# Kernel tuning notes

Hardware: AMD Instinct MI355X
Metric: run time of the kernel (lower is better)

Reference implementation:

```python
import jax, jax.numpy as jnp
import numpy as np

# FP4 (e2m1) value table: sign bit in code>>3, magnitude in code&7
FP4 = jnp.array([0.0, 0.5, 1.0, 1.5, 2.0, 3.0, 4.0, 6.0,
                 -0.0, -0.5, -1.0, -1.5, -2.0, -3.0, -4.0, -6.0], dtype=jnp.float32)
BLOCK = 32  # MX block size: one shared E8M0 scale per 32 elements


def _unpack(packed):
    # packed: int32 holding byte values 0..255; low nibble first
    lo = packed & 0xF
    hi = (packed >> 4) & 0xF
    return jnp.stack([lo, hi], axis=-1).reshape(*packed.shape[:-1], packed.shape[-1] * 2)


def _dequant(packed, sf):
    # packed: [..., N//2] packed FP4 codes; sf: [..., N//32] E8M0 exponents
    vals = FP4[_unpack(packed)]                       # [..., N]
    n = vals.shape[-1]
    scale = jnp.exp2(sf.astype(jnp.float32) - 127.0)  # [..., N//32]
    vals = vals.reshape(*vals.shape[:-1], n // BLOCK, BLOCK) * scale[..., None]
    return vals.reshape(*scale.shape[:-1], n)


def setup_inputs() -> dict:
    key = jax.random.key(0)
    ks = jax.random.split(key, 6)
    M, IN, OUT, R = 8192, 4096, 4096, 128
    return {
        "x_q": jax.random.randint(ks[0], (M, IN // 2), 0, 256, dtype=jnp.int32),
        "scales_x": jax.random.randint(ks[1], (M, IN // BLOCK), 120, 134, dtype=jnp.int32),
        "weight": jax.random.randint(ks[2], (OUT, IN // 2), 0, 256, dtype=jnp.int32),
        "SF_w": jax.random.randint(ks[3], (OUT * IN // BLOCK,), 120, 134, dtype=jnp.int32),
        "low_rank_weight": jax.random.randint(ks[4], (OUT, R // 2), 0, 256, dtype=jnp.int32),
        "SF_low_rank_weight": jax.random.randint(ks[5], (OUT * R // BLOCK,), 120, 134, dtype=jnp.int32),
    }


def reference(x_q, scales_x, weight, SF_w, low_rank_weight, SF_low_rank_weight):
    OUT = weight.shape[0]
    IN = weight.shape[1] * 2
    R = low_rank_weight.shape[1] * 2  # 128
    # Low-rank path: first R unpacked features of x (R//2 packed bytes, R//32 scale blocks)
    x_lr = _dequant(x_q[:, :R // 2], scales_x[:, :R // BLOCK])                    # [M, R]
    W_lr = _dequant(low_rank_weight, SF_low_rank_weight.reshape(OUT, R // BLOCK))  # [OUT, R]
    out = jnp.einsum('mr,or->mo', x_lr, W_lr, preferred_element_type=jnp.float32)
    # Main 4-bit matmul fused with the low-rank correction
    x = _dequant(x_q, scales_x)                               # [M, IN]
    W = _dequant(weight, SF_w.reshape(OUT, IN // BLOCK))      # [OUT, IN]
    out = out + jnp.einsum('mi,oi->mo', x, W, preferred_element_type=jnp.float32)
    return out
```

## Files before the change

kernel.cpp:

```cpp
#include <hip/hip_runtime.h>
#include <hip/hip_bf16.h>
#include <stdint.h>


#define M_DIM 8192
#define N_DIM 4096
#define K_MAIN 4096
#define K_TOT 4224
#define NCHUNK 132
#define NT 33

#define XP_OFF   ((size_t)0)
#define WP_OFF   (XP_OFF + (size_t)NCHUNK * M_DIM * 16)
#define SXH_OFF  (WP_OFF + (size_t)NCHUNK * N_DIM * 16)
#define SWH_OFF  (SXH_OFF + (size_t)NT * 2 * M_DIM * 2)
#define WS_NEED  (SWH_OFF + (size_t)NT * 2 * N_DIM * 2)

typedef __attribute__((ext_vector_type(4))) float f32x4;
typedef __attribute__((ext_vector_type(16))) float f32x16;
typedef __attribute__((ext_vector_type(8))) short short8;
typedef __attribute__((ext_vector_type(8))) _Float16 half8;
typedef __attribute__((ext_vector_type(4))) int i32x4;
typedef __attribute__((ext_vector_type(8))) int i32x8;

#define SBAR() asm volatile("s_barrier" ::: "memory")

#define PXP_N (NCHUNK * M_DIM)
#define PWP_N (NCHUNK * N_DIM)
#define TSX_N (NT * 2 * M_DIM / 2)
#define TSW_N (NT * 2 * N_DIM / 2)
#define PACK_TOTAL (PXP_N + PWP_N + TSX_N + TSW_N)

__device__ inline unsigned pack4(i32x4 q) {
    return (q.x & 255) | ((q.y & 255) << 8) | ((q.z & 255) << 16) |
           ((unsigned)(q.w & 255) << 24);
}

__global__ __launch_bounds__(256)
void pack_kernel(const int* __restrict__ xq, const int* __restrict__ sx,
                 const int* __restrict__ w, const int* __restrict__ sfw,
                 const int* __restrict__ lrw, const int* __restrict__ sflr,
                 uint8_t* __restrict__ ws) {
    int t = blockIdx.x * 256 + threadIdx.x;
    if (t < PXP_N) {
        const int g = t >> 13;
        const int m = t & 8191;
        const int gs = (g < 128) ? g : (g - 128);
        const int* src = xq + (size_t)m * 2048 + gs * 16;
        i32x4 o;
        o.x = (int)pack4(*(const i32x4*)(src + 0));
        o.y = (int)pack4(*(const i32x4*)(src + 4));
        o.z = (int)pack4(*(const i32x4*)(src + 8));
        o.w = (int)pack4(*(const i32x4*)(src + 12));
        *(i32x4*)(ws + XP_OFF + ((size_t)g * M_DIM + m) * 16) = o;
    } else if (t < PXP_N + PWP_N) {
        const int i = t - PXP_N;
        const int g = i >> 12;
        const int n = i & 4095;
        const int* src = (g < 128) ? (w + (size_t)n * 2048 + g * 16)
                                   : (lrw + (size_t)n * 64 + (g - 128) * 16);
        i32x4 o;
        o.x = (int)pack4(*(const i32x4*)(src + 0));
        o.y = (int)pack4(*(const i32x4*)(src + 4));
        o.z = (int)pack4(*(const i32x4*)(src + 8));
        o.w = (int)pack4(*(const i32x4*)(src + 12));
        *(i32x4*)(ws + WP_OFF + ((size_t)g * N_DIM + n) * 16) = o;
    } else if (t < PXP_N + PWP_N + TSX_N) {
        int i = t - PXP_N - PWP_N;
        int plane = i >> 12;
        int kt = plane >> 1, h = plane & 1;
        int r2 = (i & 4095) << 1;
        int g0 = kt * 4 + h, g2 = g0 + 2;
        int s0 = (g0 < 128) ? g0 : g0 - 128;
        int s2 = (g2 < 128) ? g2 : g2 - 128;
        unsigned b0 = sx[(size_t)r2 * 128 + s0] & 255;
        unsigned b1 = sx[(size_t)r2 * 128 + s2] & 255;
        unsigned b2 = sx[(size_t)(r2 + 1) * 128 + s0] & 255;
        unsigned b3 = sx[(size_t)(r2 + 1) * 128 + s2] & 255;
        *(unsigned*)(ws + SXH_OFF + (size_t)i * 4) = b0 | (b1 << 8) | (b2 << 16) | (b3 << 24);
    } else if (t < PACK_TOTAL) {
        int i = t - PXP_N - PWP_N - TSX_N;
        int plane = i >> 11;
        int kt = plane >> 1, h = plane & 1;
        int r2 = (i & 2047) << 1;
        int g0 = kt * 4 + h, g2 = g0 + 2;
        unsigned b0, b1, b2, b3;
        if (g0 < 128) { b0 = sfw[(size_t)r2 * 128 + g0] & 255; b2 = sfw[(size_t)(r2 + 1) * 128 + g0] & 255; }
        else          { b0 = sflr[(size_t)r2 * 4 + (g0 - 128)] & 255; b2 = sflr[(size_t)(r2 + 1) * 4 + (g0 - 128)] & 255; }
        if (g2 < 128) { b1 = sfw[(size_t)r2 * 128 + g2] & 255; b3 = sfw[(size_t)(r2 + 1) * 128 + g2] & 255; }
        else          { b1 = sflr[(size_t)r2 * 4 + (g2 - 128)] & 255; b3 = sflr[(size_t)(r2 + 1) * 4 + (g2 - 128)] & 255; }
        *(unsigned*)(ws + SWH_OFF + (size_t)i * 4) = b0 | (b1 << 8) | (b2 << 16) | (b3 << 24);
    }
}

__device__ inline void gload_lds16(const void* g, void* l) {
    __builtin_amdgcn_global_load_lds(
        (const __attribute__((address_space(1))) unsigned int*)g,
        (__attribute__((address_space(3))) unsigned int*)l, 16, 0, 0);
}

__device__ inline i32x8 ext8(i32x4 v) {
    return __builtin_shufflevector(v, v, 0, 1, 2, 3, -1, -1, -1, -1);
}

__global__ __launch_bounds__(512, 2)
void l4b_mx8(const uint8_t* __restrict__ xp, const uint8_t* __restrict__ wp,
             const uint8_t* __restrict__ sxH, const uint8_t* __restrict__ swH,
             float* __restrict__ out) {
    __shared__ __align__(16) uint8_t As[3][4][256][16];
    __shared__ __align__(16) uint8_t Bs[3][4][256][16];

    const int tid = threadIdx.x;
    const int lane = tid & 63;
    const int wid = tid >> 6;
    const int wr = wid >> 2;
    const int wc = wid & 3;

    const int bid = blockIdx.x;
    const int wgid = (bid & 7) * 64 + (bid >> 3);
    const int bn = (wgid & 15) * 256;
    const int bm = (wgid >> 4) * 256;

    const int h = lane >> 5, r = lane & 31;

    const int cst = wid & 3;
    const uint8_t* ga = (wid < 4)
        ? xp + ((size_t)cst * M_DIM + bm + lane) * 16
        : wp + ((size_t)cst * N_DIM + bn + lane) * 16;
    const size_t gstride = (wid < 4) ? (size_t)4 * M_DIM * 16 : (size_t)4 * N_DIM * 16;
    const uint8_t* psx = sxH + (size_t)(h * M_DIM + bm + wr * 128 + r) * 2;
    const uint8_t* psw = swH + (size_t)(h * N_DIM + bn + wc * 64 + r) * 2;
    const int laneoffA = h * 4096 + (wr * 128 + r) * 16;
    const int laneoffB = h * 4096 + (wc * 64 + r) * 16;

    f32x16 acc[4][2] = {};
    int sa[4], sb[2], san[4], sbn[2];

    {
        uint8_t(*T)[256][16] = (wid < 4) ? As[0] : Bs[0];
#pragma unroll
        for (int q = 0; q < 4; ++q) gload_lds16(ga + q * 1024, &T[cst][q * 64][0]);
        ga += gstride;
    }
#pragma unroll
    for (int mi = 0; mi < 4; ++mi) sa[mi] = *(const unsigned short*)(psx + mi * 64);
#pragma unroll
    for (int ni = 0; ni < 2; ++ni) sb[ni] = *(const unsigned short*)(psw + ni * 64);
    psx += 2 * M_DIM * 2;
    psw += 2 * N_DIM * 2;
    {
        uint8_t(*T)[256][16] = (wid < 4) ? As[1] : Bs[1];
#pragma unroll
        for (int q = 0; q < 4; ++q) gload_lds16(ga + q * 1024, &T[cst][q * 64][0]);
        ga += gstride;
    }
    asm volatile("s_waitcnt vmcnt(4)" ::: "memory");
    SBAR();

    int b0 = 0;
    for (int t = 0; t < NT; ++t) {
        if (t + 1 < NT) {
#pragma unroll
            for (int mi = 0; mi < 4; ++mi) san[mi] = *(const unsigned short*)(psx + mi * 64);
#pragma unroll
            for (int ni = 0; ni < 2; ++ni) sbn[ni] = *(const unsigned short*)(psw + ni * 64);
            psx += 2 * M_DIM * 2;
            psw += 2 * N_DIM * 2;
        }
        if (t + 2 < NT) {
            int b2 = b0 + 2; if (b2 >= 3) b2 -= 3;
            uint8_t(*T)[256][16] = (wid < 4) ? As[b2] : Bs[b2];
#pragma unroll
            for (int q = 0; q < 4; ++q) gload_lds16(ga + q * 1024, &T[cst][q * 64][0]);
            ga += gstride;
        }

        const char* pa = (const char*)As + b0 * 16384 + laneoffA;
        const char* pb = (const char*)Bs + b0 * 16384 + laneoffB;
        i32x4 af0[4], af1[4], bf0[2], bf1[2];
#pragma unroll
        for (int mi = 0; mi < 4; ++mi) {
            af0[mi] = *(const i32x4*)(pa + mi * 512);
            af1[mi] = *(const i32x4*)(pa + 8192 + mi * 512);
        }
#pragma unroll
        for (int ni = 0; ni < 2; ++ni) {
            bf0[ni] = *(const i32x4*)(pb + ni * 512);
            bf1[ni] = *(const i32x4*)(pb + 8192 + ni * 512);
        }

        __builtin_amdgcn_s_setprio(1);
#pragma unroll
        for (int mi = 0; mi < 4; ++mi)
#pragma unroll
            for (int ni = 0; ni < 2; ++ni)
                acc[mi][ni] = __builtin_amdgcn_mfma_scale_f32_32x32x64_f8f6f4(
                    ext8(af0[mi]), ext8(bf0[ni]), acc[mi][ni], 4, 4, 0, sa[mi], 0, sb[ni]);
#pragma unroll
        for (int mi = 0; mi < 4; ++mi)
#pragma unroll
            for (int ni = 0; ni < 2; ++ni)
                acc[mi][ni] = __builtin_amdgcn_mfma_scale_f32_32x32x64_f8f6f4(
                    ext8(af1[mi]), ext8(bf1[ni]), acc[mi][ni], 4, 4, 1, sa[mi], 1, sb[ni]);
        __builtin_amdgcn_s_setprio(0);

        if (t + 2 < NT) {
            asm volatile("s_waitcnt vmcnt(4)" ::: "memory");
        } else {
            asm volatile("s_waitcnt vmcnt(0)" ::: "memory");
        }
        SBAR();

        b0 = (b0 == 2) ? 0 : b0 + 1;
#pragma unroll
        for (int i = 0; i < 4; ++i) sa[i] = san[i];
        sb[0] = sbn[0]; sb[1] = sbn[1];
    }

#pragma unroll
    for (int mi = 0; mi < 4; ++mi)
#pragma unroll
        for (int ni = 0; ni < 2; ++ni) {
            const int col = bn + wc * 64 + ni * 32 + (lane & 31);
            const int rb = bm + wr * 128 + mi * 32 + 4 * (lane >> 5);
#pragma unroll
            for (int reg = 0; reg < 16; ++reg) {
                const int row = rb + (reg & 3) + 8 * (reg >> 2);
                out[(size_t)row * N_DIM + col] = acc[mi][ni][reg];
            }
        }
}

__device__ inline short8 dequant8_f16(i32x4 q, int sf) {
    unsigned b = (unsigned)q.x | ((unsigned)q.y << 8) |
                 ((unsigned)q.z << 16) | ((unsigned)q.w << 24);
    unsigned me = b & 0x07070707u;
    unsigned mo = (b >> 4) & 0x07070707u;
    const unsigned TLO = 0x3E3C3800u;
    const unsigned THI = 0x46444240u;
    unsigned He = __builtin_amdgcn_perm(THI, TLO, me);
    unsigned Ho = __builtin_amdgcn_perm(THI, TLO, mo);
    He |= (b & 0x08080808u) << 4;
    Ho |= (b & 0x80808080u);
    unsigned d0 = __builtin_amdgcn_perm(He, 0u, 0x05010400u);
    unsigned d1 = __builtin_amdgcn_perm(He, 0u, 0x07000600u);
    unsigned d2 = __builtin_amdgcn_perm(Ho, 0u, 0x05010400u);
    unsigned d3 = __builtin_amdgcn_perm(Ho, 0u, 0x07000600u);
    i32x4 di; di.x = (int)d0; di.y = (int)d1; di.z = (int)d2; di.w = (int)d3;
    half8 hh = __builtin_bit_cast(half8, di);
    unsigned short se = (unsigned short)((sf - 112) << 10);
    int srep = (int)((unsigned)se | ((unsigned)se << 16));
    i32x4 si; si.x = srep; si.y = srep; si.z = srep; si.w = srep;
    hh = hh * __builtin_bit_cast(half8, si);
    return __builtin_bit_cast(short8, hh);
}

__global__ __launch_bounds__(256)
void l4b_fused(const int* __restrict__ x_q, const int* __restrict__ scales_x,
               const int* __restrict__ weight, const int* __restrict__ SF_w,
               const int* __restrict__ lrw, const int* __restrict__ SF_lr,
               float* __restrict__ out) {
    __shared__ short As[128 * 64];
    __shared__ short Bs[128 * 64];
    const int tid = threadIdx.x;
    const int lane = tid & 63;
    const int wid = tid >> 6;
    const int wr = wid >> 1, wc = wid & 1;
    const int bm = blockIdx.y * 128, bn = blockIdx.x * 128;
    const int srow = tid >> 3;
    const int scol = (tid & 7) * 8;
    f32x4 acc[4][4] = {};
    for (int kt = 0; kt < K_TOT / 64; ++kt) {
        const int k0 = kt * 64;
        __syncthreads();
#pragma unroll
        for (int it = 0; it < 4; ++it) {
            const int row = it * 32 + srow;
            const int k = k0 + scol;
            const int ksrc = (k < K_MAIN) ? k : (k - K_MAIN);
            i32x4 q = *(const i32x4*)(x_q + (size_t)(bm + row) * 2048 + (ksrc >> 1));
            int sf = scales_x[(size_t)(bm + row) * 128 + (ksrc >> 5)];
            short8 v = dequant8_f16(q, sf);
            unsigned a = (unsigned)(row * 128 + scol * 2) ^ (unsigned)((row & 7) << 4);
            *(short8*)((char*)As + a) = v;
        }
#pragma unroll
        for (int it = 0; it < 4; ++it) {
            const int row = it * 32 + srow;
            const int k = k0 + scol;
            i32x4 q; int sf;
            if (k < K_MAIN) {
                q = *(const i32x4*)(weight + (size_t)(bn + row) * 2048 + (k >> 1));
                sf = SF_w[(size_t)(bn + row) * 128 + (k >> 5)];
            } else {
                q = *(const i32x4*)(lrw + (size_t)(bn + row) * 64 + ((k - K_MAIN) >> 1));
                sf = SF_lr[(size_t)(bn + row) * 4 + ((k - K_MAIN) >> 5)];
            }
            short8 v = dequant8_f16(q, sf);
            unsigned a = (unsigned)(row * 128 + scol * 2) ^ (unsigned)((row & 7) << 4);
            *(short8*)((char*)Bs + a) = v;
        }
        __syncthreads();
#pragma unroll
        for (int ks = 0; ks < 2; ++ks) {
            const int koff = ks * 32 + (lane >> 4) * 8;
            short8 af[4], bfr[4];
#pragma unroll
            for (int mi = 0; mi < 4; ++mi) {
                const int row = wr * 64 + mi * 16 + (lane & 15);
                unsigned a = (unsigned)(row * 128 + koff * 2) ^ (unsigned)((row & 7) << 4);
                af[mi] = *(const short8*)((const char*)As + a);
            }
#pragma unroll
            for (int ni = 0; ni < 4; ++ni) {
                const int row = wc * 64 + ni * 16 + (lane & 15);
                unsigned a = (unsigned)(row * 128 + koff * 2) ^ (unsigned)((row & 7) << 4);
                bfr[ni] = *(const short8*)((const char*)Bs + a);
            }
#pragma unroll
            for (int mi = 0; mi < 4; ++mi)
#pragma unroll
                for (int ni = 0; ni < 4; ++ni)
                    acc[mi][ni] = __builtin_amdgcn_mfma_f32_16x16x32_f16(
                        __builtin_bit_cast(half8, af[mi]),
                        __builtin_bit_cast(half8, bfr[ni]),
                        acc[mi][ni], 0, 0, 0);
        }
    }
#pragma unroll
    for (int mi = 0; mi < 4; ++mi)
#pragma unroll
        for (int ni = 0; ni < 4; ++ni) {
            const int col = bn + wc * 64 + ni * 16 + (lane & 15);
            const int row0 = bm + wr * 64 + mi * 16 + (lane >> 4) * 4;
#pragma unroll
            for (int r2 = 0; r2 < 4; ++r2)
                out[(size_t)(row0 + r2) * N_DIM + col] = acc[mi][ni][r2];
        }
}

extern "C" void kernel_launch(void* const* d_in, const int* in_sizes, int n_in,
                              void* d_out, int out_size, void* d_ws, size_t ws_size,
                              hipStream_t stream) {
    const int* x_q  = (const int*)d_in[0];
    const int* sx   = (const int*)d_in[1];
    const int* w    = (const int*)d_in[2];
    const int* sfw  = (const int*)d_in[3];
    const int* lrw  = (const int*)d_in[4];
    const int* sflr = (const int*)d_in[5];
    float* out = (float*)d_out;

    if (ws_size >= WS_NEED) {
        uint8_t* ws = (uint8_t*)d_ws;
        pack_kernel<<<(PACK_TOTAL + 255) / 256, 256, 0, stream>>>(x_q, sx, w, sfw, lrw, sflr, ws);
        l4b_mx8<<<(M_DIM / 256) * (N_DIM / 256), 512, 0, stream>>>(
            ws + XP_OFF, ws + WP_OFF, ws + SXH_OFF, ws + SWH_OFF, out);
    } else {
        dim3 grid(N_DIM / 128, M_DIM / 128);
        l4b_fused<<<grid, dim3(256), 0, stream>>>(x_q, sx, w, sfw, lrw, sflr, out);
    }
}
```

Before: 120.8 us.

## Double-buffer LDS fragments in registers and unroll the main loop by two

Restructures the MFMA main loop so each iteration reads the next tile's A/B fragments from LDS into a second register set while issuing the MFMAs on the current set. The loop is unrolled by two with rotating LDS buffer offsets, and the last tile is peeled after the loop. The aim is to hide LDS read latency behind matrix math. In exchange, each iteration now waits for all outstanding global-to-LDS loads (vmcnt(0)) instead of leaving the newest prefetch in flight, which may expose global latency, and the extra fragment registers raise register pressure.

```diff
diff --git a/kernel.cpp b/kernel.cpp
--- a/kernel.cpp
+++ b/kernel.cpp
@@ -103,8 +103,54 @@
     return __builtin_shufflevector(v, v, 0, 1, 2, 3, -1, -1, -1, -1);
 }
 
+struct Frags {
+    i32x4 a0[4], a1[4], b0[2], b1[2];
+};
+
+#define WINDOW(T, CUR, NXT)                                                      \
+  {                                                                              \
+    _Pragma("unroll") for (int mi = 0; mi < 4; ++mi)                             \
+        san[mi] = *(const unsigned short*)(psx + mi * 64);                       \
+    _Pragma("unroll") for (int ni = 0; ni < 2; ++ni)                             \
+        sbn[ni] = *(const unsigned short*)(psw + ni * 64);                       \
+    psx += 2 * M_DIM * 2; psw += 2 * N_DIM * 2;                                  \
+    if ((T) + 2 < NT) {                                                          \
+      char* db = ((wid < 4) ? (char*)As : (char*)Bs) + o2 + cst * 4096;          \
+      _Pragma("unroll") for (int q = 0; q < 4; ++q)                              \
+          gload_lds16(ga + q * 1024, db + q * 1024);                             \
+      ga += gstride;                                                             \
+    }                                                                            \
+    {                                                                            \
+      const char* pa = (const char*)As + o1 + laneoffA;                          \
+      const char* pb = (const char*)Bs + o1 + laneoffB;                          \
+      _Pragma("unroll") for (int mi = 0; mi < 4; ++mi) {                         \
+        NXT.a0[mi] = *(const i32x4*)(pa + mi * 512);                             \
+        NXT.a1[mi] = *(const i32x4*)(pa + 8192 + mi * 512);                      \
+      }                                                                          \
+      _Pragma("unroll") for (int ni = 0; ni < 2; ++ni) {                         \
+        NXT.b0[ni] = *(const i32x4*)(pb + ni * 512);                             \
+        NXT.b1[ni] = *(const i32x4*)(pb + 8192 + ni * 512);                      \
+      }                                                                          \
+    }                                                                            \
+    __builtin_amdgcn_s_setprio(1);                                               \
+    _Pragma("unroll") for (int mi = 0; mi < 4; ++mi)                             \
+      _Pragma("unroll") for (int ni = 0; ni < 2; ++ni)                           \
+        acc[mi][ni] = __builtin_amdgcn_mfma_scale_f32_32x32x64_f8f6f4(           \
+            ext8(CUR.a0[mi]), ext8(CUR.b0[ni]), acc[mi][ni], 4, 4, 0, sa[mi], 0, sb[ni]); \
+    _Pragma("unroll") for (int mi = 0; mi < 4; ++mi)                             \
+      _Pragma("unroll") for (int ni = 0; ni < 2; ++ni)                           \
+        acc[mi][ni] = __builtin_amdgcn_mfma_scale_f32_32x32x64_f8f6f4(           \
+            ext8(CUR.a1[mi]), ext8(CUR.b1[ni]), acc[mi][ni], 4, 4, 1, sa[mi], 1, sb[ni]); \
+    __builtin_amdgcn_s_setprio(0);                                               \
+    asm volatile("s_waitcnt vmcnt(0)" ::: "memory");                             \
+    SBAR();                                                                      \
+    int _tmp = o0; o0 = o1; o1 = o2; o2 = _tmp;                                  \
+    _Pragma("unroll") for (int i = 0; i < 4; ++i) sa[i] = san[i];                \
+    sb[0] = sbn[0]; sb[1] = sbn[1];                                              \
+  }
+
 __global__ __launch_bounds__(512, 2)
-void l4b_mx8(const uint8_t* __restrict__ xp, const uint8_t* __restrict__ wp,
+void l4b_mx9(const uint8_t* __restrict__ xp, const uint8_t* __restrict__ wp,
              const uint8_t* __restrict__ sxH, const uint8_t* __restrict__ swH,
              float* __restrict__ out) {
     __shared__ __align__(16) uint8_t As[3][4][256][16];
@@ -135,11 +181,12 @@
 
     f32x16 acc[4][2] = {};
     int sa[4], sb[2], san[4], sbn[2];
+    Frags F0, F1;
 
     {
-        uint8_t(*T)[256][16] = (wid < 4) ? As[0] : Bs[0];
-#pragma unroll
-        for (int q = 0; q < 4; ++q) gload_lds16(ga + q * 1024, &T[cst][q * 64][0]);
+        char* db = ((wid < 4) ? (char*)As : (char*)Bs) + cst * 4096;
+#pragma unroll
+        for (int q = 0; q < 4; ++q) gload_lds16(ga + q * 1024, db + q * 1024);
         ga += gstride;
     }
 #pragma unroll
@@ -149,73 +196,49 @@
     psx += 2 * M_DIM * 2;
     psw += 2 * N_DIM * 2;
     {
-        uint8_t(*T)[256][16] = (wid < 4) ? As[1] : Bs[1];
-#pragma unroll
-        for (int q = 0; q < 4; ++q) gload_lds16(ga + q * 1024, &T[cst][q * 64][0]);
+        char* db = ((wid < 4) ? (char*)As : (char*)Bs) + 16384 + cst * 4096;
+#pragma unroll
+        for (int q = 0; q < 4; ++q) gload_lds16(ga + q * 1024, db + q * 1024);
         ga += gstride;
     }
-    asm volatile("s_waitcnt vmcnt(4)" ::: "memory");
+    asm volatile("s_waitcnt vmcnt(0)" ::: "memory");
     SBAR();
-
-    int b0 = 0;
-    for (int t = 0; t < NT; ++t) {
-        if (t + 1 < NT) {
-#pragma unroll
-            for (int mi = 0; mi < 4; ++mi) san[mi] = *(const unsigned short*)(psx + mi * 64);
-#pragma unroll
-            for (int ni = 0; ni < 2; ++ni) sbn[ni] = *(const unsigned short*)(psw + ni * 64);
-            psx += 2 * M_DIM * 2;
-            psw += 2 * N_DIM * 2;
-        }
-        if (t + 2 < NT) {
-            int b2 = b0 + 2; if (b2 >= 3) b2 -= 3;
-            uint8_t(*T)[256][16] = (wid < 4) ? As[b2] : Bs[b2];
-#pragma unroll
-            for (int q = 0; q < 4; ++q) gload_lds16(ga + q * 1024, &T[cst][q * 64][0]);
-            ga += gstride;
-        }
-
-        const char* pa = (const char*)As + b0 * 16384 + laneoffA;
-        const char* pb = (const char*)Bs + b0 * 16384 + laneoffB;
-        i32x4 af0[4], af1[4], bf0[2], bf1[2];
+    {
+        const char* pa = (const char*)As + laneoffA;
+        const char* pb = (const char*)Bs + laneoffB;
 #pragma unroll
         for (int mi = 0; mi < 4; ++mi) {
-            af0[mi] = *(const i32x4*)(pa + mi * 512);
-            af1[mi] = *(const i32x4*)(pa + 8192 + mi * 512);
+            F0.a0[mi] = *(const i32x4*)(pa + mi * 512);
+            F0.a1[mi] = *(const i32x4*)(pa + 8192 + mi * 512);
         }
 #pragma unroll
         for (int ni = 0; ni < 2; ++ni) {
-            bf0[ni] = *(const i32x4*)(pb + ni * 512);
-            bf1[ni] = *(const i32x4*)(pb + 8192 + ni * 512);
-        }
-
-        __builtin_amdgcn_s_setprio(1);
-#pragma unroll
-        for (int mi = 0; mi < 4; ++mi)
-#pragma unroll
-            for (int ni = 0; ni < 2; ++ni)
-                acc[mi][ni] = __builtin_amdgcn_mfma_scale_f32_32x32x64_f8f6f4(
-                    ext8(af0[mi]), ext8(bf0[ni]), acc[mi][ni], 4, 4, 0, sa[mi], 0, sb[ni]);
-#pragma unroll
-        for (int mi = 0; mi < 4; ++mi)
-#pragma unroll
-            for (int ni = 0; ni < 2; ++ni)
-                acc[mi][ni] = __builtin_amdgcn_mfma_scale_f32_32x32x64_f8f6f4(
-                    ext8(af1[mi]), ext8(bf1[ni]), acc[mi][ni], 4, 4, 1, sa[mi], 1, sb[ni]);
-        __builtin_amdgcn_s_setprio(0);
-
-        if (t + 2 < NT) {
-            asm volatile("s_waitcnt vmcnt(4)" ::: "memory");
-        } else {
-            asm volatile("s_waitcnt vmcnt(0)" ::: "memory");
-        }
-        SBAR();
-
-        b0 = (b0 == 2) ? 0 : b0 + 1;
-#pragma unroll
-        for (int i = 0; i < 4; ++i) sa[i] = san[i];
-        sb[0] = sbn[0]; sb[1] = sbn[1];
-    }
+            F0.b0[ni] = *(const i32x4*)(pb + ni * 512);
+            F0.b1[ni] = *(const i32x4*)(pb + 8192 + ni * 512);
+        }
+    }
+
+    int o0 = 0, o1 = 16384, o2 = 32768;
+
+    for (int t = 0; t < NT - 1; t += 2) {
+        WINDOW(t, F0, F1);
+        WINDOW(t + 1, F1, F0);
+    }
+
+    __builtin_amdgcn_s_setprio(1);
+#pragma unroll
+    for (int mi = 0; mi < 4; ++mi)
+#pragma unroll
+        for (int ni = 0; ni < 2; ++ni)
+            acc[mi][ni] = __builtin_amdgcn_mfma_scale_f32_32x32x64_f8f6f4(
+                ext8(F0.a0[mi]), ext8(F0.b0[ni]), acc[mi][ni], 4, 4, 0, sa[mi], 0, sb[ni]);
+#pragma unroll
+    for (int mi = 0; mi < 4; ++mi)
+#pragma unroll
+        for (int ni = 0; ni < 2; ++ni)
+            acc[mi][ni] = __builtin_amdgcn_mfma_scale_f32_32x32x64_f8f6f4(
+                ext8(F0.a1[mi]), ext8(F0.b1[ni]), acc[mi][ni], 4, 4, 1, sa[mi], 1, sb[ni]);
+    __builtin_amdgcn_s_setprio(0);
 
 #pragma unroll
     for (int mi = 0; mi < 4; ++mi)
@@ -353,7 +376,7 @@
     if (ws_size >= WS_NEED) {
         uint8_t* ws = (uint8_t*)d_ws;
         pack_kernel<<<(PACK_TOTAL + 255) / 256, 256, 0, stream>>>(x_q, sx, w, sfw, lrw, sflr, ws);
-        l4b_mx8<<<(M_DIM / 256) * (N_DIM / 256), 512, 0, stream>>>(
+        l4b_mx9<<<(M_DIM / 256) * (N_DIM / 256), 512, 0, stream>>>(
             ws + XP_OFF, ws + WP_OFF, ws + SXH_OFF, ws + SWH_OFF, out);
     } else {
         dim3 grid(N_DIM / 128, M_DIM / 128);
```

Measured after the change: 147.0 us. 21.7% more time.
